# Kernel optimization log

Hardware: AMD Instinct MI355X
Metric: run time of the kernel (lower is better)

## Reference

```python
import jax, jax.numpy as jnp
import numpy as np

B, C_IN, HW_IN = 32, 3, 262
NUM_CLASSES = 10
GW = 64              # grid side after two conv+pool blocks: 262->260->130->128->64
N_PER = GW * GW      # 4096 nodes per image
N_NODES = B * N_PER  # 131072
E_EDGES = B * 3 * N_PER  # 393216
EPS = 1e-6
BN_EPS = 1e-5


def _build_edges():
    # Faithful replication of CGAT.build_graph edge construction (incl. its odd i*(w-1)+j indexing)
    w = h = GW
    e = []
    for i in range(w):
        for j in range(h):
            a = i * (w - 1) + j
            e.append((a, a))
            e.append((a, a + 1))
            e.append((a, i * w + j))
    e = np.asarray(e, dtype=np.int32)  # [3*n, 2]
    e = e[None, :, :] + (np.arange(B, dtype=np.int32) * N_PER)[:, None, None]
    e = e.reshape(-1, 2)
    return jnp.asarray(e[:, 0]), jnp.asarray(e[:, 1])


def _xavier(key, shape):
    fan_out, fan_in = shape[-2], shape[-1]
    lim = float(np.sqrt(6.0 / (fan_in + fan_out)))
    return jax.random.uniform(key, shape, jnp.float32, -lim, lim)


def setup_inputs() -> dict:
    key = jax.random.key(0)
    ks = iter(jax.random.split(key, 40))
    inp = {}
    inp['x'] = jax.random.normal(next(ks), (B, C_IN, HW_IN, HW_IN), jnp.float32)
    # conv block 1: Conv2d(3,32,3) + BN(32)
    inp['W1'] = jax.random.normal(next(ks), (32, C_IN, 3, 3), jnp.float32) * 0.1
    inp['b1'] = jnp.zeros((32,), jnp.float32)
    inp['g1'] = jnp.ones((32,), jnp.float32)
    inp['be1'] = jnp.zeros((32,), jnp.float32)
    # conv block 2: Conv2d(32,32,3) + BN(32)
    inp['W2'] = jax.random.normal(next(ks), (32, 32, 3, 3), jnp.float32) * 0.05
    inp['b2'] = jnp.zeros((32,), jnp.float32)
    inp['g2'] = jnp.ones((32,), jnp.float32)
    inp['be2'] = jnp.zeros((32,), jnp.float32)
    # GAT layers: sizes [32,32,64,64], heads [1,2,2,2]; head params stacked on leading axis
    # L1: d_in_eff=32 -> d_out=32, 2 heads
    inp['fW1'] = _xavier(next(ks), (2, 32, 64)); inp['fb1'] = jnp.zeros((2, 32), jnp.float32)
    inp['wW1'] = _xavier(next(ks), (2, 1, 64)); inp['wb1'] = jnp.zeros((2, 1), jnp.float32)
    # L2: d_in_eff=64 -> d_out=64, 2 heads
    inp['fW2'] = _xavier(next(ks), (2, 64, 128)); inp['fb2'] = jnp.zeros((2, 64), jnp.float32)
    inp['wW2'] = _xavier(next(ks), (2, 1, 128)); inp['wb2'] = jnp.zeros((2, 1), jnp.float32)
    # L3: d_in_eff=128 -> d_out=64, 2 heads
    inp['fW3'] = _xavier(next(ks), (2, 64, 256)); inp['fb3'] = jnp.zeros((2, 64), jnp.float32)
    inp['wW3'] = _xavier(next(ks), (2, 1, 256)); inp['wb3'] = jnp.zeros((2, 1), jnp.float32)
    # MLP head: [128, 32, num_classes]
    inp['m1W'] = _xavier(next(ks), (32, 128)); inp['m1b'] = jnp.zeros((32,), jnp.float32)
    inp['m2W'] = _xavier(next(ks), (NUM_CLASSES, 32)); inp['m2b'] = jnp.zeros((NUM_CLASSES,), jnp.float32)
    src, tgt = _build_edges()
    inp['src'] = src
    inp['tgt'] = tgt
    inp['graph_id'] = jnp.repeat(jnp.arange(B, dtype=jnp.int32), N_PER)
    return inp


def _conv_block(x, W, b, g, be):
    x = jax.lax.conv_general_dilated(x, W, (1, 1), 'VALID',
                                     dimension_numbers=('NCHW', 'OIHW', 'NCHW'))
    x = x + b[None, :, None, None]
    mu = jnp.mean(x, axis=(0, 2, 3), keepdims=True)       # BatchNorm in training mode
    var = jnp.var(x, axis=(0, 2, 3), keepdims=True)
    x = (x - mu) * jax.lax.rsqrt(var + BN_EPS) * g[None, :, None, None] + be[None, :, None, None]
    x = jax.nn.relu(x)
    return jax.lax.reduce_window(x, -jnp.inf, jax.lax.max, (1, 1, 2, 2), (1, 1, 2, 2), 'VALID')


def _gat_layer(x, src, tgt, fW, fb, wW, wb):
    # x: [N, d_in_eff]; fW: [H, f, 2d]; wW: [H, 1, 2d]
    n = x.shape[0]
    h = jnp.concatenate([x[src], x[tgt]], axis=1)                    # [E, 2d] gather
    y = jax.nn.relu(jnp.einsum('ed,hfd->ehf', h, fW) + fb[None])     # [E, H, f]
    a = jnp.einsum('ed,hod->eho', h, wW) + wb[None]                  # [E, H, 1]
    a_exp = jnp.exp(a - jnp.max(a, axis=0, keepdims=True))           # global max, per head (as torch)
    # Mtgt @ v  ==  segment_sum(v, tgt)  (edge-softmax denominator/numerator)
    a_sum = jax.ops.segment_sum(a_exp, tgt, num_segments=n) + EPS    # [N, H, 1]
    o = jax.ops.segment_sum(y * a_exp, tgt, num_segments=n) / a_sum  # [N, H, f]
    return o.reshape(n, -1)                                          # concat heads


def _forward(x, W1, b1, g1, be1, W2, b2, g2, be2,
             fW1, fb1, wW1, wb1, fW2, fb2, wW2, wb2, fW3, fb3, wW3, wb3,
             m1W, m1b, m2W, m2b, src, tgt, graph_id):
    x = _conv_block(x, W1, b1, g1, be1)
    x = _conv_block(x, W2, b2, g2, be2)   # [B, 32, 64, 64]
    b, c = x.shape[0], x.shape[1]
    x = x.reshape(b, c, -1).transpose(0, 2, 1).reshape(-1, c)  # [N, 32]
    x = _gat_layer(x, src, tgt, fW1, fb1, wW1, wb1)  # [N, 64]
    x = _gat_layer(x, src, tgt, fW2, fb2, wW2, wb2)  # [N, 128]
    x = _gat_layer(x, src, tgt, fW3, fb3, wW3, wb3)  # [N, 128]
    x = jax.ops.segment_sum(x, graph_id, num_segments=B)  # Mgraph^T @ x -> [B, 128]
    x = jax.nn.relu(x @ m1W.T + m1b)
    return x @ m2W.T + m2b


def reference(x, W1, b1, g1, be1, W2, b2, g2, be2,
              fW1, fb1, wW1, wb1, fW2, fb2, wW2, wb2, fW3, fb3, wW3, wb3,
              m1W, m1b, m2W, m2b, src, tgt, graph_id):
    return _forward(x, W1, b1, g1, be1, W2, b2, g2, be2,
                    fW1, fb1, wW1, wb1, fW2, fb2, wW2, wb2, fW3, fb3, wW3, wb3,
                    m1W, m1b, m2W, m2b, src, tgt, graph_id)
```

## Files before the change

### kernel.cpp

```cpp
#include <hip/hip_runtime.h>
#include <math.h>

#define NNODES  131072
#define NEDGES  393216

static const size_t OFF_X     = 0;
static const size_t OFF_U     = 16777216;
static const size_t OFF_PA    = OFF_U + 16777216;
static const size_t OFF_GPOOL = OFF_PA;
static const size_t OFF_V     = OFF_U + 17305600;
static const size_t OFF_AEXP  = OFF_V + 16777216;
static const size_t OFF_CUR   = OFF_AEXP + 786432;
static const size_t OFF_CSRE  = OFF_CUR + 131072;
static const size_t OFF_WUV   = OFF_CSRE + 393216;
static const size_t OFF_UB    = OFF_WUV + 32768;
static const size_t OFF_STATS = OFF_UB + 128;
static const size_t OFF_SS    = OFF_STATS + 128;
static const size_t OFF_AMAX  = OFF_SS + 64;

__device__ inline unsigned enc_f(float f) {
  int b = __float_as_int(f);
  unsigned u = (unsigned)b;
  return (b >= 0) ? (u | 0x80000000u) : ~u;
}
__device__ inline float dec_f(unsigned e) {
  unsigned b = (e & 0x80000000u) ? (e & 0x7FFFFFFFu) : ~e;
  return __int_as_float((int)b);
}

__global__ void repackW1_k(const float* __restrict__ W1, float* __restrict__ W1T) {
  int i = blockIdx.x * 256 + threadIdx.x;
  if (i >= 864) return;
  int j = i >> 5, c = i & 31;
  W1T[i] = W1[c * 27 + j];
}

__global__ void repackW2_k(const float* __restrict__ W2, float* __restrict__ W2T) {
  int i = blockIdx.x * 256 + threadIdx.x;
  if (i >= 9216) return;
  int j = i >> 5, c = i & 31;
  W2T[i] = W2[c * 288 + j];
}

__global__ __launch_bounds__(256) void conv1_tiled_k(const float* __restrict__ x,
    const float* __restrict__ W1T, const float* __restrict__ b1,
    float* __restrict__ PR1, float* __restrict__ part) {
  __shared__ float in_t[972];
  __shared__ float rs1[256], rs2[256];
  int tx = blockIdx.x, ty = blockIdx.y, b = blockIdx.z;
  int tid = threadIdx.x;
  int r0 = 16 * ty, c0 = 16 * tx;
  for (int idx = tid; idx < 972; idx += 256) {
    int ci = idx / 324, rc = idx - ci * 324;
    int row = rc / 18, col = rc - row * 18;
    int gr = r0 + row, gc = c0 + col;
    float v = 0.f;
    if (gr < 262 && gc < 262) v = x[(size_t)(b * 3 + ci) * 68644 + gr * 262 + gc];
    in_t[idx] = v;
  }
  __syncthreads();
  int c = tid & 31, pg = tid >> 5;
  float w[27];
#pragma unroll
  for (int j = 0; j < 27; ++j) w[j] = W1T[j * 32 + c];
  float bias = b1[c];
  int px = tx * 8 + pg;
  float s1 = 0.f, s2 = 0.f;
#pragma unroll
  for (int r = 0; r < 8; ++r) {
    int py = ty * 8 + r;
    if (py < 130 && px < 130) {
      float a00 = bias, a01 = bias, a10 = bias, a11 = bias;
#pragma unroll
      for (int ci = 0; ci < 3; ++ci) {
        const float* ip = &in_t[ci * 324 + (2 * r) * 18 + 2 * pg];
#pragma unroll
        for (int dy = 0; dy < 3; ++dy) {
#pragma unroll
          for (int dx = 0; dx < 3; ++dx) {
            float wv = w[ci * 9 + dy * 3 + dx];
            a00 += ip[dy * 18 + dx]           * wv;
            a01 += ip[dy * 18 + dx + 1]       * wv;
            a10 += ip[(dy + 1) * 18 + dx]     * wv;
            a11 += ip[(dy + 1) * 18 + dx + 1] * wv;
          }
        }
      }
      s1 += a00 + a01 + a10 + a11;
      s2 += a00 * a00 + a01 * a01 + a10 * a10 + a11 * a11;
      float m = fmaxf(fmaxf(a00, a01), fmaxf(a10, a11));
      PR1[((size_t)b * 16900 + py * 130 + px) * 32 + c] = m;
    }
  }
  rs1[tid] = s1; rs2[tid] = s2;
  __syncthreads();
  if (tid < 32) {
    float a = 0.f, q = 0.f;
    for (int g = 0; g < 8; ++g) { a += rs1[g * 32 + tid]; q += rs2[g * 32 + tid]; }
    int bid = (b * 17 + ty) * 17 + tx;
    part[(size_t)bid * 64 + tid * 2 + 0] = a;
    part[(size_t)bid * 64 + tid * 2 + 1] = q;
  }
}

__global__ void stats_reduce_k(const float* __restrict__ part, double* __restrict__ stats, int nb) {
  __shared__ double sd[256];
  int cnt = blockIdx.x;
  double s = 0.0;
  for (int b = threadIdx.x; b < nb; b += 256) s += (double)part[(size_t)b * 64 + cnt];
  sd[threadIdx.x] = s;
  __syncthreads();
  for (int o = 128; o > 0; o >>= 1) { if (threadIdx.x < o) sd[threadIdx.x] += sd[threadIdx.x + o]; __syncthreads(); }
  if (threadIdx.x == 0) stats[cnt] = sd[0];
}

__global__ void bn_finalize_k(const double* __restrict__ stats, const float* __restrict__ g,
                              const float* __restrict__ be, float* __restrict__ ss, double inv_cnt) {
  int c = threadIdx.x;
  if (c < 32) {
    double mu  = stats[c * 2 + 0] * inv_cnt;
    double var = stats[c * 2 + 1] * inv_cnt - mu * mu;
    double scale = (double)g[c] / sqrt(var + 1e-5);
    ss[c]      = (float)scale;
    ss[32 + c] = (float)((double)be[c] - mu * scale);
  }
}

__global__ __launch_bounds__(256) void conv2_tiled_k(const float* __restrict__ pool1,
    const float* __restrict__ ss, const float* __restrict__ W2T, const float* __restrict__ b2,
    float* __restrict__ PR2, float* __restrict__ part) {
  __shared__ float in_t[5184];
  __shared__ float rs1[256], rs2[256];
  __shared__ float ssl[64];
  int tx = blockIdx.x, ty = blockIdx.y, b = blockIdx.z;
  int tid = threadIdx.x;
  if (tid < 64) ssl[tid] = ss[tid];
  int r0 = 16 * ty, c0 = 16 * tx;
  const float* pb = pool1 + ((size_t)b * 16900 + r0 * 130 + c0) * 32;
  int c = tid & 31, pg = tid >> 5;
  float bias = b2[c];
  float acc[8][4];
#pragma unroll
  for (int r = 0; r < 8; ++r) { acc[r][0] = bias; acc[r][1] = bias; acc[r][2] = bias; acc[r][3] = bias; }
  int cb = 2 * pg;
#pragma unroll 1
  for (int ph = 0; ph < 2; ++ph) {
    __syncthreads();
    int cib = ph * 16;
    for (int idx = tid; idx < 5184; idx += 256) {
      int rc = idx >> 4, ci16 = idx & 15;
      int row = rc / 18, col = rc - row * 18;
      int ci = cib + ci16;
      float v = pb[(size_t)(row * 130 + col) * 32 + ci];
      in_t[idx] = fmaxf(v * ssl[ci] + ssl[32 + ci], 0.f);
    }
    __syncthreads();
#pragma unroll 1
    for (int ci16 = 0; ci16 < 16; ++ci16) {
      int ci = cib + ci16;
      float w[9];
#pragma unroll
      for (int k = 0; k < 9; ++k) w[k] = W2T[(ci * 9 + k) * 32 + c];
      float r0v[4], r1v[4], r2v[4], r3v[4];
#pragma unroll
      for (int q = 0; q < 4; ++q) {
        r0v[q] = in_t[(0 * 18 + cb + q) * 16 + ci16];
        r1v[q] = in_t[(1 * 18 + cb + q) * 16 + ci16];
      }
#pragma unroll
      for (int r = 0; r < 8; ++r) {
#pragma unroll
        for (int q = 0; q < 4; ++q) {
          r2v[q] = in_t[((2 * r + 2) * 18 + cb + q) * 16 + ci16];
          r3v[q] = in_t[((2 * r + 3) * 18 + cb + q) * 16 + ci16];
        }
#pragma unroll
        for (int dx = 0; dx < 3; ++dx) {
          float w0 = w[dx], w1 = w[3 + dx], w2 = w[6 + dx];
          acc[r][0] += r0v[dx]     * w0 + r1v[dx]     * w1 + r2v[dx]     * w2;
          acc[r][1] += r0v[dx + 1] * w0 + r1v[dx + 1] * w1 + r2v[dx + 1] * w2;
          acc[r][2] += r1v[dx]     * w0 + r2v[dx]     * w1 + r3v[dx]     * w2;
          acc[r][3] += r1v[dx + 1] * w0 + r2v[dx + 1] * w1 + r3v[dx + 1] * w2;
        }
#pragma unroll
        for (int q = 0; q < 4; ++q) { r0v[q] = r2v[q]; r1v[q] = r3v[q]; }
      }
    }
  }
  float s1 = 0.f, s2 = 0.f;
  int px = tx * 8 + pg;
#pragma unroll
  for (int r = 0; r < 8; ++r) {
    s1 += acc[r][0] + acc[r][1] + acc[r][2] + acc[r][3];
    s2 += acc[r][0] * acc[r][0] + acc[r][1] * acc[r][1] + acc[r][2] * acc[r][2] + acc[r][3] * acc[r][3];
    int py = ty * 8 + r;
    float m = fmaxf(fmaxf(acc[r][0], acc[r][1]), fmaxf(acc[r][2], acc[r][3]));
    PR2[((size_t)b * 4096 + py * 64 + px) * 32 + c] = m;
  }
  rs1[tid] = s1; rs2[tid] = s2;
  __syncthreads();
  if (tid < 32) {
    float a = 0.f, q = 0.f;
    for (int g = 0; g < 8; ++g) { a += rs1[g * 32 + tid]; q += rs2[g * 32 + tid]; }
    int bid = (b * 8 + ty) * 8 + tx;
    part[(size_t)bid * 64 + tid * 2 + 0] = a;
    part[(size_t)bid * 64 + tid * 2 + 1] = q;
  }
}

__global__ void bn_relu2_k(const float* __restrict__ PR2, const float* __restrict__ ss,
                           float* __restrict__ X) {
  int i = blockIdx.x * 256 + threadIdx.x;
  int c = i & 31;
  X[i] = fmaxf(PR2[i] * ss[c] + ss[32 + c], 0.f);
}

__global__ void deg_k(const int* __restrict__ tgt, int* __restrict__ cur) {
  int e = blockIdx.x * 256 + threadIdx.x;
  atomicAdd(&cur[tgt[e]], 1);
}

__global__ void scan_k(int* __restrict__ cur) {
  __shared__ int ls[1024];
  int tid = threadIdx.x;
  int base = tid * 128;
  int sum = 0;
  for (int i = 0; i < 128; ++i) sum += cur[base + i];
  ls[tid] = sum;
  __syncthreads();
  for (int off = 1; off < 1024; off <<= 1) {
    int v = (tid >= off) ? ls[tid - off] : 0;
    __syncthreads();
    ls[tid] += v;
    __syncthreads();
  }
  int excl = ls[tid] - sum;
  for (int i = 0; i < 128; ++i) { int d = cur[base + i]; cur[base + i] = excl; excl += d; }
}

__global__ void scatter_k(const int* __restrict__ tgt, int* __restrict__ cur,
                          int* __restrict__ csre) {
  int e = blockIdx.x * 256 + threadIdx.x;
  int t = tgt[e];
  int pos = atomicAdd(&cur[t], 1);
  csre[pos] = e;
}

__global__ void repack2_k(const float* __restrict__ fW, const float* __restrict__ fb,
                          float* __restrict__ WUV, float* __restrict__ UB,
                          unsigned* __restrict__ amax, int D, int HF) {
  int NN = 2 * HF, D2 = 2 * D;
  int i = blockIdx.x * 256 + threadIdx.x;
  if (i < 2) amax[i] = 0x007FFFFFu;
  if (i < HF) UB[i] = fb[i];
  if (i >= D * NN) return;
  int k = i / NN, j = i - k * NN;
  int half = (j >= HF) ? 1 : 0;
  int cc = j - half * HF;
  WUV[i] = fW[(size_t)cc * D2 + half * D + k];
}

__global__ __launch_bounds__(256) void gemm_uv_k(const float* __restrict__ X,
    const float* __restrict__ WUV, const float* __restrict__ UB,
    float* __restrict__ U, float* __restrict__ V, int D, int HF) {
  const int NN = 2 * HF;
  __shared__ float As[16][132];
  __shared__ float Bs[16][68];
  int tid = threadIdx.x;
  int tx = tid & 15, ty = tid >> 4;
  int rm = blockIdx.y * 128;
  int cn = blockIdx.x * 64;
  float acc[8][4] = {};
  int ar = tid >> 1;
  int ak = (tid & 1) * 8;
  int bk = tid >> 4;
  int bj = (tid & 15) * 4;
  for (int kb = 0; kb < D; kb += 16) {
    const float* xr = &X[(size_t)(rm + ar) * D + kb + ak];
    float4 a0 = *(const float4*)&xr[0];
    float4 a1 = *(const float4*)&xr[4];
    float4 bv = *(const float4*)&WUV[(size_t)(kb + bk) * NN + cn + bj];
    __syncthreads();
    As[ak + 0][ar] = a0.x; As[ak + 1][ar] = a0.y; As[ak + 2][ar] = a0.z; As[ak + 3][ar] = a0.w;
    As[ak + 4][ar] = a1.x; As[ak + 5][ar] = a1.y; As[ak + 6][ar] = a1.z; As[ak + 7][ar] = a1.w;
    *(float4*)&Bs[bk][bj] = bv;
    __syncthreads();
#pragma unroll
    for (int k = 0; k < 16; ++k) {
      float4 am0 = *(float4*)&As[k][ty * 8];
      float4 am1 = *(float4*)&As[k][ty * 8 + 4];
      float4 b = *(float4*)&Bs[k][tx * 4];
      acc[0][0] += am0.x * b.x; acc[0][1] += am0.x * b.y; acc[0][2] += am0.x * b.z; acc[0][3] += am0.x * b.w;
      acc[1][0] += am0.y * b.x; acc[1][1] += am0.y * b.y; acc[1][2] += am0.y * b.z; acc[1][3] += am0.y * b.w;
      acc[2][0] += am0.z * b.x; acc[2][1] += am0.z * b.y; acc[2][2] += am0.z * b.z; acc[2][3] += am0.z * b.w;
      acc[3][0] += am0.w * b.x; acc[3][1] += am0.w * b.y; acc[3][2] += am0.w * b.z; acc[3][3] += am0.w * b.w;
      acc[4][0] += am1.x * b.x; acc[4][1] += am1.x * b.y; acc[4][2] += am1.x * b.z; acc[4][3] += am1.x * b.w;
      acc[5][0] += am1.y * b.x; acc[5][1] += am1.y * b.y; acc[5][2] += am1.y * b.z; acc[5][3] += am1.y * b.w;
      acc[6][0] += am1.z * b.x; acc[6][1] += am1.z * b.y; acc[6][2] += am1.z * b.z; acc[6][3] += am1.z * b.w;
      acc[7][0] += am1.w * b.x; acc[7][1] += am1.w * b.y; acc[7][2] += am1.w * b.z; acc[7][3] += am1.w * b.w;
    }
  }
  bool isU = (cn < HF);
  float4 ub = make_float4(0.f, 0.f, 0.f, 0.f);
  if (isU) ub = *(const float4*)&UB[cn + tx * 4];
  float* dstBase = isU ? (U + cn) : (V + (cn - HF));
#pragma unroll
  for (int i = 0; i < 8; ++i) {
    int row = rm + ty * 8 + i;
    float4 o = make_float4(acc[i][0] + ub.x, acc[i][1] + ub.y, acc[i][2] + ub.z, acc[i][3] + ub.w);
    *(float4*)&dstBase[(size_t)row * HF + tx * 4] = o;
  }
}

__global__ void pvec_k(const float* __restrict__ X, const float* __restrict__ wW,
                       const float* __restrict__ wb, float* __restrict__ PA, int D) {
  __shared__ float PWs[4 * 132];
  int tid = threadIdx.x;
  int D2 = 2 * D;
  for (int i = tid; i < 4 * D; i += 64) {
    int v = i / D, k = i - v * D;
    PWs[v * 132 + k] = (v < 2) ? wW[v * D2 + k] : wW[(v - 2) * D2 + D + k];
  }
  __syncthreads();
  int v = tid & 3;
  int n = blockIdx.x * 16 + (tid >> 2);
  const float* xr = X + (size_t)n * D;
  float acc = 0.f;
  for (int k = 0; k < D; k += 4) {
    float4 xv = *(const float4*)&xr[k];
    acc += xv.x * PWs[v * 132 + k] + xv.y * PWs[v * 132 + k + 1]
         + xv.z * PWs[v * 132 + k + 2] + xv.w * PWs[v * 132 + k + 3];
  }
  if (v < 2) acc += wb[v];
  PA[(size_t)n * 4 + v] = acc;
}

__global__ void edge_logit_k(const int* __restrict__ src, const int* __restrict__ tgt,
                             const float* __restrict__ PA, float* __restrict__ aexp,
                             unsigned* __restrict__ amax) {
  int e = blockIdx.x * 256 + threadIdx.x;
  int s = src[e], t = tgt[e];
  float4 ps = *(const float4*)&PA[(size_t)s * 4];
  float4 pt = *(const float4*)&PA[(size_t)t * 4];
  float a0 = ps.x + pt.z;
  float a1 = ps.y + pt.w;
  aexp[e * 2 + 0] = a0;
  aexp[e * 2 + 1] = a1;
#pragma unroll
  for (int o = 32; o > 0; o >>= 1) {
    a0 = fmaxf(a0, __shfl_down(a0, o));
    a1 = fmaxf(a1, __shfl_down(a1, o));
  }
  if ((threadIdx.x & 63) == 0) {
    atomicMax(&amax[0], enc_f(a0));
    atomicMax(&amax[1], enc_f(a1));
  }
}

__global__ void gather_k(const int* __restrict__ cur, const int* __restrict__ csre,
                         const int* __restrict__ src, const float* __restrict__ aexp,
                         const unsigned* __restrict__ amax,
                         const float* __restrict__ U, const float* __restrict__ V,
                         float* __restrict__ X, int HF, int F, int lq) {
  int tid = blockIdx.x * 256 + threadIdx.x;
  int r4 = tid & ((HF >> 2) - 1);
  int t = tid >> lq;
  int r0 = r4 << 2;
  int h = (r0 >= F) ? 1 : 0;
  float mh = dec_f(amax[h]);
  int start = (t == 0) ? 0 : cur[t - 1];
  int end = cur[t];
  float4 v4 = *(const float4*)&V[(size_t)t * HF + r0];
  float ax = 0.f, ay = 0.f, az = 0.f, aw = 0.f, den = 0.f;
  for (int e = start; e < end; ++e) {
    int eo = csre[e];
    int s = src[eo];
    float ae = __expf(aexp[(size_t)eo * 2 + h] - mh);
    den += ae;
    const float4 u4 = *(const float4*)&U[(size_t)s * HF + r0];
    ax += ae * fmaxf(u4.x + v4.x, 0.f);
    ay += ae * fmaxf(u4.y + v4.y, 0.f);
    az += ae * fmaxf(u4.z + v4.z, 0.f);
    aw += ae * fmaxf(u4.w + v4.w, 0.f);
  }
  float inv = 1.f / (den + 1e-6f);
  float4 o = make_float4(ax * inv, ay * inv, az * inv, aw * inv);
  *(float4*)&X[(size_t)t * HF + r0] = o;
}

__global__ void graph_pool_k(const float* __restrict__ X, float* __restrict__ gp) {
  int g = blockIdx.y, chunk = blockIdx.x, j = threadIdx.x;
  int base = g * 4096 + chunk * 128;
  float acc = 0.f;
  for (int i = 0; i < 128; ++i) acc += X[(size_t)(base + i) * 128 + j];
  atomicAdd(&gp[g * 128 + j], acc);
}

__global__ void mlp_k(const float* __restrict__ gp, const float* __restrict__ m1W,
                      const float* __restrict__ m1b, const float* __restrict__ m2W,
                      const float* __restrict__ m2b, float* __restrict__ out) {
  __shared__ float hid[1024];
  int tid = threadIdx.x;
  int g = tid >> 5, j = tid & 31;
  float acc = m1b[j];
  for (int k = 0; k < 128; ++k) acc += gp[g * 128 + k] * m1W[j * 128 + k];
  hid[g * 32 + j] = fmaxf(acc, 0.f);
  __syncthreads();
  if (tid < 320) {
    int gg = tid / 10, c2 = tid - gg * 10;
    float o = m2b[c2];
    for (int k = 0; k < 32; ++k) o += hid[gg * 32 + k] * m2W[c2 * 32 + k];
    out[gg * 10 + c2] = o;
  }
}

extern "C" void kernel_launch(void* const* d_in, const int* in_sizes, int n_in,
                              void* d_out, int out_size, void* d_ws, size_t ws_size,
                              hipStream_t stream) {
  (void)in_sizes; (void)n_in; (void)out_size; (void)ws_size;
  const float* x   = (const float*)d_in[0];
  const float* W1  = (const float*)d_in[1];
  const float* b1  = (const float*)d_in[2];
  const float* g1  = (const float*)d_in[3];
  const float* be1 = (const float*)d_in[4];
  const float* W2  = (const float*)d_in[5];
  const float* b2  = (const float*)d_in[6];
  const float* g2  = (const float*)d_in[7];
  const float* be2 = (const float*)d_in[8];
  const int* src = (const int*)d_in[25];
  const int* tgt = (const int*)d_in[26];

  float* ws = (float*)d_ws;
  float* X     = ws + OFF_X;
  float* PR1   = ws + OFF_U;
  float* U     = ws + OFF_U;
  float* V     = ws + OFF_V;
  float* AEXP  = ws + OFF_AEXP;
  float* PA    = ws + OFF_PA;
  int*   CUR   = (int*)(ws + OFF_CUR);
  int*   CSRE  = (int*)(ws + OFF_CSRE);
  float* WUV   = ws + OFF_WUV;
  float* UB    = ws + OFF_UB;
  double* STATS= (double*)(ws + OFF_STATS);
  float* SS    = ws + OFF_SS;
  float* GPOOL = ws + OFF_GPOOL;
  unsigned* AMAX = (unsigned*)(ws + OFF_AMAX);
  float* PART  = X;
  float* W1T   = X + 1000000;
  float* W2T   = X + 1001000;

  repackW1_k<<<4, 256, 0, stream>>>(W1, W1T);
  repackW2_k<<<36, 256, 0, stream>>>(W2, W2T);

  conv1_tiled_k<<<dim3(17, 17, 32), 256, 0, stream>>>(x, W1T, b1, PR1, PART);
  stats_reduce_k<<<64, 256, 0, stream>>>(PART, STATS, 9248);
  bn_finalize_k<<<1, 64, 0, stream>>>(STATS, g1, be1, SS, 1.0 / 2163200.0);

  conv2_tiled_k<<<dim3(8, 8, 32), 256, 0, stream>>>(PR1, SS, W2T, b2, V, PART);
  stats_reduce_k<<<64, 256, 0, stream>>>(PART, STATS, 2048);
  bn_finalize_k<<<1, 64, 0, stream>>>(STATS, g2, be2, SS, 1.0 / 524288.0);
  bn_relu2_k<<<16384, 256, 0, stream>>>(V, SS, X);

  hipMemsetAsync(CUR, 0, NNODES * sizeof(int), stream);
  deg_k<<<NEDGES / 256, 256, 0, stream>>>(tgt, CUR);
  scan_k<<<1, 1024, 0, stream>>>(CUR);
  scatter_k<<<NEDGES / 256, 256, 0, stream>>>(tgt, CUR, CSRE);

  for (int l = 0; l < 3; ++l) {
    int D  = (l == 0) ? 32 : (l == 1) ? 64 : 128;
    int F  = (l == 0) ? 32 : 64;
    int HF = 2 * F, NN = 2 * HF;
    int lq = (l == 0) ? 4 : 5;
    const float* fW = (const float*)d_in[9  + l * 4];
    const float* fb = (const float*)d_in[10 + l * 4];
    const float* wW = (const float*)d_in[11 + l * 4];
    const float* wb = (const float*)d_in[12 + l * 4];

    repack2_k<<<(D * NN + 255) / 256, 256, 0, stream>>>(fW, fb, WUV, UB, AMAX, D, HF);
    gemm_uv_k<<<dim3(NN / 64, NNODES / 128), 256, 0, stream>>>(X, WUV, UB, U, V, D, HF);
    pvec_k<<<NNODES / 16, 64, 0, stream>>>(X, wW, wb, PA, D);
    edge_logit_k<<<NEDGES / 256, 256, 0, stream>>>(src, tgt, PA, AEXP, AMAX);
    gather_k<<<(NNODES * (HF / 4)) / 256, 256, 0, stream>>>(CUR, CSRE, src, AEXP, AMAX, U, V, X, HF, F, lq);
  }

  hipMemsetAsync(GPOOL, 0, 4096 * sizeof(float), stream);
  graph_pool_k<<<dim3(32, 32), 128, 0, stream>>>(X, GPOOL);
  mlp_k<<<1, 1024, 0, stream>>>(GPOOL, (const float*)d_in[21], (const float*)d_in[22],
                                (const float*)d_in[23], (const float*)d_in[24], (float*)d_out);
}
```

Baseline: 1.327 ms.

## Transpose conv2 shared tile to channel-major and precompute edge exponentials

```diff
diff --git a/kernel.cpp b/kernel.cpp
--- a/kernel.cpp
+++ b/kernel.cpp
@@ -129,7 +129,7 @@
 __global__ __launch_bounds__(256) void conv2_tiled_k(const float* __restrict__ pool1,
     const float* __restrict__ ss, const float* __restrict__ W2T, const float* __restrict__ b2,
     float* __restrict__ PR2, float* __restrict__ part) {
-  __shared__ float in_t[5184];
+  __shared__ float in_t[16 * 326];
   __shared__ float rs1[256], rs2[256];
   __shared__ float ssl[64];
   int tx = blockIdx.x, ty = blockIdx.y, b = blockIdx.z;
@@ -150,9 +150,8 @@
     for (int idx = tid; idx < 5184; idx += 256) {
       int rc = idx >> 4, ci16 = idx & 15;
       int row = rc / 18, col = rc - row * 18;
-      int ci = cib + ci16;
-      float v = pb[(size_t)(row * 130 + col) * 32 + ci];
-      in_t[idx] = fmaxf(v * ssl[ci] + ssl[32 + ci], 0.f);
+      float v = pb[(size_t)(row * 130 + col) * 32 + cib + ci16];
+      in_t[ci16 * 326 + rc] = fmaxf(v * ssl[cib + ci16] + ssl[32 + cib + ci16], 0.f);
     }
     __syncthreads();
 #pragma unroll 1
@@ -161,19 +160,18 @@
       float w[9];
 #pragma unroll
       for (int k = 0; k < 9; ++k) w[k] = W2T[(ci * 9 + k) * 32 + c];
+      const float* bt = &in_t[ci16 * 326 + cb];
       float r0v[4], r1v[4], r2v[4], r3v[4];
-#pragma unroll
-      for (int q = 0; q < 4; ++q) {
-        r0v[q] = in_t[(0 * 18 + cb + q) * 16 + ci16];
-        r1v[q] = in_t[(1 * 18 + cb + q) * 16 + ci16];
-      }
+      *(float2*)&r0v[0] = *(const float2*)&bt[0 * 18 + 0];
+      *(float2*)&r0v[2] = *(const float2*)&bt[0 * 18 + 2];
+      *(float2*)&r1v[0] = *(const float2*)&bt[1 * 18 + 0];
+      *(float2*)&r1v[2] = *(const float2*)&bt[1 * 18 + 2];
 #pragma unroll
       for (int r = 0; r < 8; ++r) {
-#pragma unroll
-        for (int q = 0; q < 4; ++q) {
-          r2v[q] = in_t[((2 * r + 2) * 18 + cb + q) * 16 + ci16];
-          r3v[q] = in_t[((2 * r + 3) * 18 + cb + q) * 16 + ci16];
-        }
+        *(float2*)&r2v[0] = *(const float2*)&bt[(2 * r + 2) * 18 + 0];
+        *(float2*)&r2v[2] = *(const float2*)&bt[(2 * r + 2) * 18 + 2];
+        *(float2*)&r3v[0] = *(const float2*)&bt[(2 * r + 3) * 18 + 0];
+        *(float2*)&r3v[2] = *(const float2*)&bt[(2 * r + 3) * 18 + 2];
 #pragma unroll
         for (int dx = 0; dx < 3; ++dx) {
           float w0 = w[dx], w1 = w[3 + dx], w2 = w[6 + dx];
@@ -357,9 +355,17 @@
   }
 }
 
+__global__ void edge_exp_k(float* __restrict__ aexp, const unsigned* __restrict__ amax) {
+  int e = blockIdx.x * 256 + threadIdx.x;
+  float m0 = dec_f(amax[0]), m1 = dec_f(amax[1]);
+  float2 lg = *(float2*)&aexp[e * 2];
+  lg.x = __expf(lg.x - m0);
+  lg.y = __expf(lg.y - m1);
+  *(float2*)&aexp[e * 2] = lg;
+}
+
 __global__ void gather_k(const int* __restrict__ cur, const int* __restrict__ csre,
                          const int* __restrict__ src, const float* __restrict__ aexp,
-                         const unsigned* __restrict__ amax,
                          const float* __restrict__ U, const float* __restrict__ V,
                          float* __restrict__ X, int HF, int F, int lq) {
   int tid = blockIdx.x * 256 + threadIdx.x;
@@ -367,7 +373,6 @@
   int t = tid >> lq;
   int r0 = r4 << 2;
   int h = (r0 >= F) ? 1 : 0;
-  float mh = dec_f(amax[h]);
   int start = (t == 0) ? 0 : cur[t - 1];
   int end = cur[t];
   float4 v4 = *(const float4*)&V[(size_t)t * HF + r0];
@@ -375,7 +380,7 @@
   for (int e = start; e < end; ++e) {
     int eo = csre[e];
     int s = src[eo];
-    float ae = __expf(aexp[(size_t)eo * 2 + h] - mh);
+    float ae = aexp[(size_t)eo * 2 + h];
     den += ae;
     const float4 u4 = *(const float4*)&U[(size_t)s * HF + r0];
     ax += ae * fmaxf(u4.x + v4.x, 0.f);
@@ -480,7 +485,8 @@
     gemm_uv_k<<<dim3(NN / 64, NNODES / 128), 256, 0, stream>>>(X, WUV, UB, U, V, D, HF);
     pvec_k<<<NNODES / 16, 64, 0, stream>>>(X, wW, wb, PA, D);
     edge_logit_k<<<NEDGES / 256, 256, 0, stream>>>(src, tgt, PA, AEXP, AMAX);
-    gather_k<<<(NNODES * (HF / 4)) / 256, 256, 0, stream>>>(CUR, CSRE, src, AEXP, AMAX, U, V, X, HF, F, lq);
+    edge_exp_k<<<NEDGES / 256, 256, 0, stream>>>(AEXP, AMAX);
+    gather_k<<<(NNODES * (HF / 4)) / 256, 256, 0, stream>>>(CUR, CSRE, src, AEXP, U, V, X, HF, F, lq);
   }
 
   hipMemsetAsync(GPOOL, 0, 4096 * sizeof(float), stream);
```

After: 1.341 ms. Within noise of the previous version (+1.0%).
